# Kernel optimization log

Hardware: AMD Instinct MI355X
Metric: run time of the kernel (lower is better)

## Reference

```python
import jax, jax.numpy as jnp
import numpy as np

N = 100000      # nodes
E = 640000      # edges
IN = 100        # in_channels
OUT = 128       # out_channels
H, D = 4, 32    # heads, per-head dim (OUT = H*D)
MSG, TOUT, ETD, NET = 16, 100, 8, 4
EDGE_COLS = MSG + TOUT + 2        # 118 raw edge_attr columns
EDIM = (MSG - 1) + ETD + TOUT + 2 # 125 processed edge feature dim
SCALE = 1.0 / np.sqrt(D)


def _lin(k, fi, fo):
    return (jax.random.normal(k, (fi, fo), jnp.float32) / np.sqrt(fi)).astype(jnp.float32)


def setup_inputs() -> dict:
    key = jax.random.key(0)
    ks = jax.random.split(key, 24)
    x = jax.random.normal(ks[0], (N, IN), jnp.float32)
    edge_index = jax.random.randint(ks[1], (2, E), 0, N, dtype=jnp.int32)
    ea = jax.random.normal(ks[2], (E, EDGE_COLS), jnp.float32)
    etype = jax.random.randint(ks[3], (E,), 0, NET).astype(jnp.float32)
    edge_attr = ea.at[:, 3].set(etype)
    emb = jax.random.normal(ks[4], (NET, ETD), jnp.float32)
    inp = {"x": x, "edge_index": edge_index, "edge_attr": edge_attr, "emb": emb}
    # conv1: in=IN, conv2: in=OUT; lin_edge has no bias (PyG default)
    for i, fi in ((1, IN), (2, OUT)):
        base = 5 + (i - 1) * 8
        inp[f"w{i}q"] = _lin(ks[base + 0], fi, OUT)
        inp[f"b{i}q"] = jnp.zeros((OUT,), jnp.float32)
        inp[f"w{i}k"] = _lin(ks[base + 1], fi, OUT)
        inp[f"b{i}k"] = jnp.zeros((OUT,), jnp.float32)
        inp[f"w{i}v"] = _lin(ks[base + 2], fi, OUT)
        inp[f"b{i}v"] = jnp.zeros((OUT,), jnp.float32)
        inp[f"w{i}e"] = _lin(ks[base + 3], EDIM, OUT)
        inp[f"w{i}s"] = _lin(ks[base + 4], fi, OUT)
        inp[f"b{i}s"] = jnp.zeros((OUT,), jnp.float32)
    return inp


def _seg_softmax(logits, seg, n):
    # logits: [E, H], softmax over edges sharing the same target node
    m = jax.ops.segment_max(logits, seg, num_segments=n)      # [N, H]
    ex = jnp.exp(logits - m[seg])
    s = jax.ops.segment_sum(ex, seg, num_segments=n)          # [N, H]
    return ex / (s[seg] + 1e-16)


def _tconv(x, src, dst, e, wq, bq, wk, bk, wv, bv, we, ws, bs):
    n = x.shape[0]
    q = (x @ wq + bq)[dst].reshape(-1, H, D)   # gather targets
    k = (x @ wk + bk)[src].reshape(-1, H, D)   # gather sources
    v = (x @ wv + bv)[src].reshape(-1, H, D)
    ee = (e @ we).reshape(-1, H, D)            # per-edge projection
    alpha = jnp.sum(q * (k + ee), axis=-1) * SCALE          # [E, H]
    a = _seg_softmax(alpha, dst, n)                          # scatter-softmax
    msg = (v + ee) * a[..., None]                            # [E, H, D]
    out = jax.ops.segment_sum(msg, dst, num_segments=n).reshape(n, H * D)
    return out + x @ ws + bs                                 # root/skip connection


def reference(x, edge_index, edge_attr, emb,
              w1q, b1q, w1k, b1k, w1v, b1v, w1e, w1s, b1s,
              w2q, b2q, w2k, b2k, w2v, b2v, w2e, w2s, b2s):
    src, dst = edge_index[0], edge_index[1]
    cont = edge_attr[:, :3]
    etype = edge_attr[:, 3].astype(jnp.int32)
    rest = edge_attr[:, 4:]
    e = jnp.concatenate([cont, rest, emb[etype]], axis=-1)   # [E, EDIM]
    h = jax.nn.relu(_tconv(x, src, dst, e, w1q, b1q, w1k, b1k, w1v, b1v, w1e, w1s, b1s))
    return _tconv(h, src, dst, e, w2q, b2q, w2k, b2k, w2v, b2v, w2e, w2s, b2s)
```

## Files before the change

kernel.cpp:

```cpp
#include <hip/hip_runtime.h>

#define NN 100000
#define NE 640000
#define OUTF 128
#define K1 100
#define KE 118
#define KPAD 128
#define ASTR 136
#define ATT_SCALE 0.17677669529663687f
#define NTILE 5000
#define NSCANB 391

typedef __attribute__((ext_vector_type(8))) short short8;
typedef __attribute__((ext_vector_type(4))) float f32x4;

__device__ __forceinline__ unsigned short f2bf(float f) {
    unsigned u = __float_as_uint(f);
    u += 0x7FFFu + ((u >> 16) & 1u);
    return (unsigned short)(u >> 16);
}
__device__ __forceinline__ float bf2f(unsigned short h) {
    return __uint_as_float(((unsigned)h) << 16);
}

__global__ void prep_weights(
    const float* __restrict__ w1q, const float* __restrict__ w1k,
    const float* __restrict__ w1v, const float* __restrict__ w1s,
    const float* __restrict__ w2q, const float* __restrict__ w2k,
    const float* __restrict__ w2v, const float* __restrict__ w2s,
    const float* __restrict__ we1, const float* __restrict__ we2,
    const float* __restrict__ emb,
    const float* __restrict__ b1q, const float* __restrict__ b1k,
    const float* __restrict__ b1v, const float* __restrict__ b1s,
    const float* __restrict__ b2q, const float* __restrict__ b2k,
    const float* __restrict__ b2v, const float* __restrict__ b2s,
    unsigned short* __restrict__ WT1, unsigned short* __restrict__ WT2,
    unsigned short* __restrict__ WmT1, unsigned short* __restrict__ WmT2,
    float* __restrict__ bias1, float* __restrict__ bias2)
{
    int idx = blockIdx.x * blockDim.x + threadIdx.x;
    int stride = gridDim.x * blockDim.x;
    for (int i = idx; i < 512 * KPAD; i += stride) {
        int col = i >> 7, k = i & 127;
        int which = col >> 7, c = col & 127;
        const float* s1 = (which == 0) ? w1q : (which == 1) ? w1k : (which == 2) ? w1v : w1s;
        const float* s2 = (which == 0) ? w2q : (which == 1) ? w2k : (which == 2) ? w2v : w2s;
        float v1 = (k < K1) ? s1[k * OUTF + c] : 0.f;
        float v2 = s2[k * OUTF + c];
        WT1[i] = f2bf(v1); WT2[i] = f2bf(v2);
    }
    for (int i = idx; i < OUTF * KPAD; i += stride) {
        int col = i >> 7, k = i & 127;
        float v1 = 0.f, v2 = 0.f;
        if (k < 3)                 { v1 = we1[k * OUTF + col];       v2 = we2[k * OUTF + col]; }
        else if (k >= 4 && k < KE) { v1 = we1[(k - 1) * OUTF + col]; v2 = we2[(k - 1) * OUTF + col]; }
        else if (k >= KE && k < KE + 4) {
            int t = k - KE;
            #pragma unroll
            for (int r = 0; r < 8; r++) {
                float ev = emb[t * 8 + r];
                v1 += ev * we1[(117 + r) * OUTF + col];
                v2 += ev * we2[(117 + r) * OUTF + col];
            }
        }
        WmT1[i] = f2bf(v1); WmT2[i] = f2bf(v2);
    }
    for (int i = idx; i < 512; i += stride) {
        int which = i >> 7, c = i & 127;
        const float* sb1 = (which == 0) ? b1q : (which == 1) ? b1k : (which == 2) ? b1v : b1s;
        const float* sb2 = (which == 0) ? b2q : (which == 1) ? b2k : (which == 2) ? b2v : b2s;
        bias1[i] = sb1[c]; bias2[i] = sb2[c];
    }
}

__global__ __launch_bounds__(256) void prep_edges(const float* __restrict__ EA,
                                                  const int* __restrict__ dstI,
                                                  unsigned short* __restrict__ EAp,
                                                  int* __restrict__ cnt, int do_hist)
{
    __shared__ unsigned short Alds[128][ASTR];
    __shared__ int et_lds[128];
    int tid = threadIdx.x;
    int tile = blockIdx.x;
    int e0 = tile * 128;

    for (int idx = tid; idx < 128 * 64; idx += 256) {
        int r = idx >> 6, slot = idx & 63;
        int k = slot * 2;
        float2 v = make_float2(0.f, 0.f);
        if (k < KE) v = *(const float2*)(EA + (size_t)(e0 + r) * KE + k);
        if (slot == 1) { et_lds[r] = (int)v.y; v.y = 0.f; }
        unsigned pv = (unsigned)f2bf(v.x) | ((unsigned)f2bf(v.y) << 16);
        *(unsigned*)&Alds[r][k] = pv;
    }
    __syncthreads();
    if (tid < 128) {
        Alds[tid][KE + et_lds[tid]] = 0x3F80;
        if (do_hist) atomicAdd(&cnt[dstI[e0 + tid]], 1);
    }
    __syncthreads();
    size_t base = (size_t)tile * 16384;
    #pragma unroll
    for (int it = 0; it < 8; it++) {
        int cid = it * 256 + tid;
        int g = cid >> 8, ks = (cid >> 6) & 3, l15 = (cid >> 2) & 15, l4 = cid & 3;
        uint4 v = *(const uint4*)&Alds[g * 16 + l15][ks * 32 + l4 * 8];
        *(uint4*)(EAp + base + (size_t)cid * 8) = v;
    }
}

__global__ void scan1(const int* __restrict__ cnt, int* __restrict__ S1, int* __restrict__ bsum) {
    __shared__ int sd[256];
    int t = blockIdx.x * 256 + threadIdx.x;
    sd[threadIdx.x] = (t < NN) ? cnt[t] : 0;
    __syncthreads();
    for (int off = 1; off < 256; off <<= 1) {
        int x = (threadIdx.x >= off) ? sd[threadIdx.x - off] : 0;
        __syncthreads();
        sd[threadIdx.x] += x;
        __syncthreads();
    }
    if (t < NN) S1[t] = sd[threadIdx.x];
    if (threadIdx.x == 255) bsum[blockIdx.x] = sd[255];
}
__global__ void scan2(const int* __restrict__ bsum, int* __restrict__ boff) {
    __shared__ int sd[512];
    int t = threadIdx.x;
    sd[t] = (t < NSCANB) ? bsum[t] : 0;
    __syncthreads();
    for (int off = 1; off < 512; off <<= 1) {
        int x = (t >= off) ? sd[t - off] : 0;
        __syncthreads();
        sd[t] += x;
        __syncthreads();
    }
    if (t < NSCANB) boff[t] = (t == 0) ? 0 : sd[t - 1];
}
__global__ void scan3(const int* __restrict__ S1, const int* __restrict__ boff,
                      const int* __restrict__ cnt,
                      int* __restrict__ row_start, int* __restrict__ cursor) {
    int t = blockIdx.x * 256 + threadIdx.x;
    if (t < NN) {
        int incl = S1[t] + boff[t >> 8];
        row_start[t + 1] = incl;
        cursor[t] = incl - cnt[t];
        if (t == 0) row_start[0] = 0;
    }
}
__global__ void scatter_csr(const int* __restrict__ srcI, const int* __restrict__ dstI,
                            int* __restrict__ cursor,
                            int* __restrict__ csr_src, int* __restrict__ csr_eid) {
    int e = blockIdx.x * 256 + threadIdx.x;
    if (e < NE) {
        int j = atomicAdd(&cursor[dstI[e]], 1);
        csr_src[j] = srcI[e];
        csr_eid[j] = e;
    }
}

__global__ __launch_bounds__(256) void node_mfma(
    const float* __restrict__ X, int ldx, int Kdim, int relu, int n,
    const unsigned short* __restrict__ WT, const float* __restrict__ bias,
    float* __restrict__ Y0, float* __restrict__ Y1,
    float* __restrict__ Y2, float* __restrict__ Y3,
    int ld012, int ld3)
{
    __shared__ unsigned short Alds[128][ASTR];
    int tid = threadIdx.x;
    int rowbase = blockIdx.x * 128;

    for (int idx = tid; idx < 128 * 68; idx += 256) {
        int r = idx / 68, kv = idx % 68;
        int k = kv * 2;
        float2 v = make_float2(0.f, 0.f);
        int gr = rowbase + r;
        if (gr < n && k < Kdim) v = *(const float2*)(X + (size_t)gr * ldx + k);
        if (relu) { v.x = fmaxf(v.x, 0.f); v.y = fmaxf(v.y, 0.f); }
        unsigned pv = (unsigned)f2bf(v.x) | ((unsigned)f2bf(v.y) << 16);
        *(unsigned*)&Alds[r][k] = pv;
    }
    __syncthreads();

    int lane = tid & 63, wid = tid >> 6;
    int wm = wid >> 1, wn = wid & 1;
    int l15 = lane & 15, l4 = lane >> 4;

    for (int nb = 0; nb < 4; nb++) {
        f32x4 acc[4][4];
        #pragma unroll
        for (int mf = 0; mf < 4; mf++)
            #pragma unroll
            for (int nf = 0; nf < 4; nf++)
                acc[mf][nf] = (f32x4){0.f, 0.f, 0.f, 0.f};

        const unsigned short* wbase = WT + (size_t)(nb * 128 + wn * 64 + l15) * KPAD + l4 * 8;
        #pragma unroll
        for (int ks = 0; ks < 4; ks++) {
            short8 af[4], bfr[4];
            #pragma unroll
            for (int mf = 0; mf < 4; mf++)
                af[mf] = *(const short8*)&Alds[wm * 64 + mf * 16 + l15][ks * 32 + l4 * 8];
            #pragma unroll
            for (int nf = 0; nf < 4; nf++)
                bfr[nf] = *(const short8*)(wbase + (size_t)nf * 16 * KPAD + ks * 32);
            #pragma unroll
            for (int mf = 0; mf < 4; mf++)
                #pragma unroll
                for (int nf = 0; nf < 4; nf++)
                    acc[mf][nf] = __builtin_amdgcn_mfma_f32_16x16x32_bf16(af[mf], bfr[nf], acc[mf][nf], 0, 0, 0);
        }

        float* Yb = (nb == 0) ? Y0 : (nb == 1) ? Y1 : (nb == 2) ? Y2 : Y3;
        int ld = (nb == 3) ? ld3 : ld012;
        #pragma unroll
        for (int nf = 0; nf < 4; nf++) {
            int col = wn * 64 + nf * 16 + l15;
            float bv = bias[nb * 128 + col];
            #pragma unroll
            for (int mf = 0; mf < 4; mf++) {
                #pragma unroll
                for (int rr = 0; rr < 4; rr++) {
                    int row = rowbase + wm * 64 + mf * 16 + l4 * 4 + rr;
                    if (row < n) Yb[(size_t)row * ld + col] = acc[mf][nf][rr] + bv;
                }
            }
        }
    }
}

__global__ __launch_bounds__(256) void edge_mfma(unsigned short* EAp,
                                                 const unsigned short* __restrict__ WmT)
{
    __shared__ unsigned short Slds[128][ASTR];
    int tid = threadIdx.x;
    int tile = blockIdx.x;
    int lane = tid & 63, wm = tid >> 6;
    int l15 = lane & 15, l4 = lane >> 4;
    size_t base = (size_t)tile * 16384;

    short8 af[2][4];
    #pragma unroll
    for (int mf = 0; mf < 2; mf++)
        #pragma unroll
        for (int ks = 0; ks < 4; ks++) {
            int g = wm * 2 + mf;
            int cid = ((g * 4 + ks) * 16 + l15) * 4 + l4;
            af[mf][ks] = *(const short8*)(EAp + base + (size_t)cid * 8);
        }

    f32x4 acc[2][8];
    #pragma unroll
    for (int mf = 0; mf < 2; mf++)
        #pragma unroll
        for (int nf = 0; nf < 8; nf++)
            acc[mf][nf] = (f32x4){0.f, 0.f, 0.f, 0.f};

    #pragma unroll
    for (int ks = 0; ks < 4; ks++) {
        short8 bfr[8];
        #pragma unroll
        for (int nf = 0; nf < 8; nf++)
            bfr[nf] = *(const short8*)(WmT + (size_t)(nf * 16 + l15) * KPAD + ks * 32 + l4 * 8);
        #pragma unroll
        for (int mf = 0; mf < 2; mf++)
            #pragma unroll
            for (int nf = 0; nf < 8; nf++)
                acc[mf][nf] = __builtin_amdgcn_mfma_f32_16x16x32_bf16(af[mf][ks], bfr[nf], acc[mf][nf], 0, 0, 0);
    }

    #pragma unroll
    for (int mf = 0; mf < 2; mf++)
        #pragma unroll
        for (int nf = 0; nf < 8; nf++)
            #pragma unroll
            for (int rr = 0; rr < 4; rr++)
                Slds[wm * 32 + mf * 16 + l4 * 4 + rr][nf * 16 + l15] = f2bf(acc[mf][nf][rr]);
    __syncthreads();

    #pragma unroll
    for (int it = 0; it < 8; it++) {
        int cid = it * 256 + tid;
        int row = cid >> 4, c8 = (cid & 15) * 8;
        uint4 v = *(const uint4*)&Slds[row][c8];
        *(uint4*)(EAp + base + (size_t)row * 128 + c8) = v;
    }
}

__global__ __launch_bounds__(256) void attn_node(
    const float* __restrict__ Y,
    const unsigned short* __restrict__ EE,
    const int* __restrict__ row_start,
    const int* __restrict__ csr_src, const int* __restrict__ csr_eid,
    const float* __restrict__ Hsrc, int ldh,
    float* __restrict__ Out, int ldo)
{
    int lane = threadIdx.x & 63;
    int gw = (int)((blockIdx.x * (size_t)blockDim.x + threadIdx.x) >> 6);
    int nW = (gridDim.x * blockDim.x) >> 6;
    int c2 = lane * 2;

    for (int d = gw; d < NN; d += nW) {
        int rs = row_start[d], re = row_start[d + 1];
        float2 q = *(const float2*)(Y + (size_t)d * 512 + c2);
        float m = -3.4e38f, s = 0.f, a0 = 0.f, a1 = 0.f;
        for (int j = rs; j < re; j++) {
            int sj = csr_src[j], ej = csr_eid[j];
            float2 kv = *(const float2*)(Y + (size_t)sj * 512 + 128 + c2);
            float2 vv = *(const float2*)(Y + (size_t)sj * 512 + 256 + c2);
            unsigned eeb = *(const unsigned*)(EE + (size_t)ej * 128 + c2);
            float e0 = bf2f((unsigned short)(eeb & 0xFFFFu));
            float e1 = bf2f((unsigned short)(eeb >> 16));
            float t = q.x * (kv.x + e0) + q.y * (kv.y + e1);
            t += __shfl_xor(t, 1); t += __shfl_xor(t, 2);
            t += __shfl_xor(t, 4); t += __shfl_xor(t, 8);
            float alpha = t * ATT_SCALE;
            float mn = fmaxf(m, alpha);
            float r = __expf(m - mn);
            float p = __expf(alpha - mn);
            s = s * r + p;
            a0 = a0 * r + p * (vv.x + e0);
            a1 = a1 * r + p * (vv.y + e1);
            m = mn;
        }
        float inv = 1.f / (s + 1e-16f);
        float2 h = *(const float2*)(Hsrc + (size_t)d * ldh + c2);
        float2 o;
        o.x = a0 * inv + h.x;
        o.y = a1 * inv + h.y;
        *(float2*)(Out + (size_t)d * ldo + c2) = o;
    }
}

extern "C" void kernel_launch(void* const* d_in, const int* in_sizes, int n_in,
                              void* d_out, int out_size, void* d_ws, size_t ws_size,
                              hipStream_t stream) {
    const float* x    = (const float*)d_in[0];
    const int*   ei   = (const int*)d_in[1];
    const float* ea   = (const float*)d_in[2];
    const float* emb  = (const float*)d_in[3];
    const float* w1q  = (const float*)d_in[4];  const float* b1q = (const float*)d_in[5];
    const float* w1k  = (const float*)d_in[6];  const float* b1k = (const float*)d_in[7];
    const float* w1v  = (const float*)d_in[8];  const float* b1v = (const float*)d_in[9];
    const float* w1e  = (const float*)d_in[10];
    const float* w1s  = (const float*)d_in[11]; const float* b1s = (const float*)d_in[12];
    const float* w2q  = (const float*)d_in[13]; const float* b2q = (const float*)d_in[14];
    const float* w2k  = (const float*)d_in[15]; const float* b2k = (const float*)d_in[16];
    const float* w2v  = (const float*)d_in[17]; const float* b2v = (const float*)d_in[18];
    const float* w2e  = (const float*)d_in[19];
    const float* w2s  = (const float*)d_in[20]; const float* b2s = (const float*)d_in[21];

    const int* srcI = ei;
    const int* dstI = ei + NE;

    float* Y = (float*)d_ws;
    unsigned short* EAp = (unsigned short*)(Y + (size_t)NN * 512);
    int* csr_src   = (int*)(EAp + (size_t)NE * 128);
    int* csr_eid   = csr_src + NE;
    int* row_start = csr_eid + NE;
    int* cursor    = row_start + NN + 1;
    int* cnt       = cursor + NN;
    int* S1        = cnt + NN;
    int* bsum      = S1 + NN;
    int* boff      = bsum + NSCANB;
    unsigned short* WT1  = (unsigned short*)(boff + NSCANB + 1);
    unsigned short* WT2  = WT1 + 512 * KPAD;
    unsigned short* WmT1 = WT2 + 512 * KPAD;
    unsigned short* WmT2 = WmT1 + OUTF * KPAD;
    float* bias1 = (float*)(WmT2 + OUTF * KPAD);
    float* bias2 = bias1 + 512;

    prep_weights<<<128, 256, 0, stream>>>(w1q, w1k, w1v, w1s, w2q, w2k, w2v, w2s,
                                          w1e, w2e, emb,
                                          b1q, b1k, b1v, b1s, b2q, b2k, b2v, b2s,
                                          WT1, WT2, WmT1, WmT2, bias1, bias2);
    hipMemsetAsync(cnt, 0, (size_t)NN * sizeof(int), stream);
    prep_edges<<<NTILE, 256, 0, stream>>>(ea, dstI, EAp, cnt, 1);
    scan1<<<NSCANB, 256, 0, stream>>>(cnt, S1, bsum);
    scan2<<<1, 512, 0, stream>>>(bsum, boff);
    scan3<<<NSCANB, 256, 0, stream>>>(S1, boff, cnt, row_start, cursor);
    scatter_csr<<<NE / 256, 256, 0, stream>>>(srcI, dstI, cursor, csr_src, csr_eid);

    int ngrid = (NN + 127) / 128;

    node_mfma<<<ngrid, 256, 0, stream>>>(x, K1, K1, 0, NN, WT1, bias1,
                                         Y + 0, Y + 128, Y + 256, Y + 384, 512, 512);
    edge_mfma<<<NTILE, 256, 0, stream>>>(EAp, WmT1);
    attn_node<<<2048, 256, 0, stream>>>(Y, EAp, row_start, csr_src, csr_eid,
                                        Y + 384, 512, Y + 384, 512);

    node_mfma<<<ngrid, 256, 0, stream>>>(Y + 384, 512, OUTF, 1, NN, WT2, bias2,
                                         Y + 0, Y + 128, Y + 256, (float*)d_out, 512, 128);
    prep_edges<<<NTILE, 256, 0, stream>>>(ea, dstI, EAp, cnt, 0);
    edge_mfma<<<NTILE, 256, 0, stream>>>(EAp, WmT2);
    attn_node<<<2048, 256, 0, stream>>>(Y, EAp, row_start, csr_src, csr_eid,
                                        (float*)d_out, 128, (float*)d_out, 128);
}
```

Measured before the change: 1.162 ms.

## Fuse edge prep into dual-layer edge GEMM, store K/V bf16, CSR-order edge features

Replaces the two prep_edges plus edge_mfma passes with a single kernel that reads raw edge attributes once and computes both layers' edge projections, writing them directly in CSR (destination-sorted) order via a per-edge position array. K and V node projections are now stored as bf16 in an interleaved buffer, and Q and skip are kept in separate compact fp32 arrays. The attention loop drops the csr_eid indirection, reads edge features contiguously, and software-prefetches the next edge's K/V/E. This removes a re-read of the fp32 edge attributes and halves gather bytes for K/V, at the cost of a second edge-feature buffer, scattered writes, and extra bf16 rounding of K/V.

```diff
diff --git a/kernel.cpp b/kernel.cpp
--- a/kernel.cpp
+++ b/kernel.cpp
@@ -73,42 +73,10 @@
     }
 }
 
-__global__ __launch_bounds__(256) void prep_edges(const float* __restrict__ EA,
-                                                  const int* __restrict__ dstI,
-                                                  unsigned short* __restrict__ EAp,
-                                                  int* __restrict__ cnt, int do_hist)
-{
-    __shared__ unsigned short Alds[128][ASTR];
-    __shared__ int et_lds[128];
-    int tid = threadIdx.x;
-    int tile = blockIdx.x;
-    int e0 = tile * 128;
-
-    for (int idx = tid; idx < 128 * 64; idx += 256) {
-        int r = idx >> 6, slot = idx & 63;
-        int k = slot * 2;
-        float2 v = make_float2(0.f, 0.f);
-        if (k < KE) v = *(const float2*)(EA + (size_t)(e0 + r) * KE + k);
-        if (slot == 1) { et_lds[r] = (int)v.y; v.y = 0.f; }
-        unsigned pv = (unsigned)f2bf(v.x) | ((unsigned)f2bf(v.y) << 16);
-        *(unsigned*)&Alds[r][k] = pv;
-    }
-    __syncthreads();
-    if (tid < 128) {
-        Alds[tid][KE + et_lds[tid]] = 0x3F80;
-        if (do_hist) atomicAdd(&cnt[dstI[e0 + tid]], 1);
-    }
-    __syncthreads();
-    size_t base = (size_t)tile * 16384;
-    #pragma unroll
-    for (int it = 0; it < 8; it++) {
-        int cid = it * 256 + tid;
-        int g = cid >> 8, ks = (cid >> 6) & 3, l15 = (cid >> 2) & 15, l4 = cid & 3;
-        uint4 v = *(const uint4*)&Alds[g * 16 + l15][ks * 32 + l4 * 8];
-        *(uint4*)(EAp + base + (size_t)cid * 8) = v;
-    }
-}
-
+__global__ void hist_kernel(const int* __restrict__ dstI, int* __restrict__ cnt) {
+    int e = blockIdx.x * 256 + threadIdx.x;
+    if (e < NE) atomicAdd(&cnt[dstI[e]], 1);
+}
 __global__ void scan1(const int* __restrict__ cnt, int* __restrict__ S1, int* __restrict__ bsum) {
     __shared__ int sd[256];
     int t = blockIdx.x * 256 + threadIdx.x;
@@ -149,21 +117,19 @@
 }
 __global__ void scatter_csr(const int* __restrict__ srcI, const int* __restrict__ dstI,
                             int* __restrict__ cursor,
-                            int* __restrict__ csr_src, int* __restrict__ csr_eid) {
+                            int* __restrict__ csr_src, int* __restrict__ epos) {
     int e = blockIdx.x * 256 + threadIdx.x;
     if (e < NE) {
         int j = atomicAdd(&cursor[dstI[e]], 1);
         csr_src[j] = srcI[e];
-        csr_eid[j] = e;
+        epos[e] = j;
     }
 }
 
 __global__ __launch_bounds__(256) void node_mfma(
     const float* __restrict__ X, int ldx, int Kdim, int relu, int n,
     const unsigned short* __restrict__ WT, const float* __restrict__ bias,
-    float* __restrict__ Y0, float* __restrict__ Y1,
-    float* __restrict__ Y2, float* __restrict__ Y3,
-    int ld012, int ld3)
+    float* __restrict__ Qp, unsigned short* __restrict__ KVp, float* __restrict__ Hp)
 {
     __shared__ unsigned short Alds[128][ASTR];
     int tid = threadIdx.x;
@@ -210,8 +176,6 @@
                     acc[mf][nf] = __builtin_amdgcn_mfma_f32_16x16x32_bf16(af[mf], bfr[nf], acc[mf][nf], 0, 0, 0);
         }
 
-        float* Yb = (nb == 0) ? Y0 : (nb == 1) ? Y1 : (nb == 2) ? Y2 : Y3;
-        int ld = (nb == 3) ? ld3 : ld012;
         #pragma unroll
         for (int nf = 0; nf < 4; nf++) {
             int col = wn * 64 + nf * 16 + l15;
@@ -221,78 +185,100 @@
                 #pragma unroll
                 for (int rr = 0; rr < 4; rr++) {
                     int row = rowbase + wm * 64 + mf * 16 + l4 * 4 + rr;
-                    if (row < n) Yb[(size_t)row * ld + col] = acc[mf][nf][rr] + bv;
+                    if (row < n) {
+                        float val = acc[mf][nf][rr] + bv;
+                        if (nb == 0)      Qp[(size_t)row * OUTF + col] = val;
+                        else if (nb == 3) Hp[(size_t)row * OUTF + col] = val;
+                        else KVp[(size_t)row * 256 + (nb == 1 ? 0 : 128) + col] = f2bf(val);
+                    }
                 }
             }
         }
     }
 }
 
-__global__ __launch_bounds__(256) void edge_mfma(unsigned short* EAp,
-                                                 const unsigned short* __restrict__ WmT)
+__global__ __launch_bounds__(256) void edge_mfma_dual(
+    const float* __restrict__ EA, const int* __restrict__ epos,
+    const unsigned short* __restrict__ WmT1, const unsigned short* __restrict__ WmT2,
+    unsigned short* __restrict__ EE1, unsigned short* __restrict__ EE2)
 {
-    __shared__ unsigned short Slds[128][ASTR];
+    __shared__ unsigned short Alds[128][ASTR];
+    __shared__ int et_lds[128];
+    __shared__ int pos_lds[128];
     int tid = threadIdx.x;
-    int tile = blockIdx.x;
+    int e0 = blockIdx.x * 128;
+
+    for (int idx = tid; idx < 128 * 64; idx += 256) {
+        int r = idx >> 6, slot = idx & 63;
+        int k = slot * 2;
+        float2 v = make_float2(0.f, 0.f);
+        if (k < KE) v = *(const float2*)(EA + (size_t)(e0 + r) * KE + k);
+        if (slot == 1) { et_lds[r] = (int)v.y; v.y = 0.f; }
+        unsigned pv = (unsigned)f2bf(v.x) | ((unsigned)f2bf(v.y) << 16);
+        *(unsigned*)&Alds[r][k] = pv;
+    }
+    __syncthreads();
+    if (tid < 128) {
+        Alds[tid][KE + et_lds[tid]] = 0x3F80;
+        pos_lds[tid] = epos[e0 + tid];
+    }
+    __syncthreads();
+
     int lane = tid & 63, wm = tid >> 6;
     int l15 = lane & 15, l4 = lane >> 4;
-    size_t base = (size_t)tile * 16384;
 
     short8 af[2][4];
     #pragma unroll
     for (int mf = 0; mf < 2; mf++)
         #pragma unroll
+        for (int ks = 0; ks < 4; ks++)
+            af[mf][ks] = *(const short8*)&Alds[wm * 32 + mf * 16 + l15][ks * 32 + l4 * 8];
+
+    auto do_layer = [&](const unsigned short* __restrict__ WmT, unsigned short* __restrict__ EEc) {
+        f32x4 acc[2][8];
+        #pragma unroll
+        for (int mf = 0; mf < 2; mf++)
+            #pragma unroll
+            for (int nf = 0; nf < 8; nf++)
+                acc[mf][nf] = (f32x4){0.f, 0.f, 0.f, 0.f};
+
+        #pragma unroll
         for (int ks = 0; ks < 4; ks++) {
-            int g = wm * 2 + mf;
-            int cid = ((g * 4 + ks) * 16 + l15) * 4 + l4;
-            af[mf][ks] = *(const short8*)(EAp + base + (size_t)cid * 8);
-        }
-
-    f32x4 acc[2][8];
-    #pragma unroll
-    for (int mf = 0; mf < 2; mf++)
-        #pragma unroll
-        for (int nf = 0; nf < 8; nf++)
-            acc[mf][nf] = (f32x4){0.f, 0.f, 0.f, 0.f};
-
-    #pragma unroll
-    for (int ks = 0; ks < 4; ks++) {
-        short8 bfr[8];
-        #pragma unroll
-        for (int nf = 0; nf < 8; nf++)
-            bfr[nf] = *(const short8*)(WmT + (size_t)(nf * 16 + l15) * KPAD + ks * 32 + l4 * 8);
+            short8 bfr[8];
+            #pragma unroll
+            for (int nf = 0; nf < 8; nf++)
+                bfr[nf] = *(const short8*)(WmT + (size_t)(nf * 16 + l15) * KPAD + ks * 32 + l4 * 8);
+            #pragma unroll
+            for (int mf = 0; mf < 2; mf++)
+                #pragma unroll
+                for (int nf = 0; nf < 8; nf++)
+                    acc[mf][nf] = __builtin_amdgcn_mfma_f32_16x16x32_bf16(af[mf][ks], bfr[nf], acc[mf][nf], 0, 0, 0);
+        }
         #pragma unroll
         for (int mf = 0; mf < 2; mf++)
             #pragma unroll
             for (int nf = 0; nf < 8; nf++)
-                acc[mf][nf] = __builtin_amdgcn_mfma_f32_16x16x32_bf16(af[mf][ks], bfr[nf], acc[mf][nf], 0, 0, 0);
-    }
-
-    #pragma unroll
-    for (int mf = 0; mf < 2; mf++)
-        #pragma unroll
-        for (int nf = 0; nf < 8; nf++)
-            #pragma unroll
-            for (int rr = 0; rr < 4; rr++)
-                Slds[wm * 32 + mf * 16 + l4 * 4 + rr][nf * 16 + l15] = f2bf(acc[mf][nf][rr]);
-    __syncthreads();
-
-    #pragma unroll
-    for (int it = 0; it < 8; it++) {
-        int cid = it * 256 + tid;
-        int row = cid >> 4, c8 = (cid & 15) * 8;
-        uint4 v = *(const uint4*)&Slds[row][c8];
-        *(uint4*)(EAp + base + (size_t)row * 128 + c8) = v;
-    }
+                #pragma unroll
+                for (int rr = 0; rr < 4; rr++)
+                    Alds[wm * 32 + mf * 16 + l4 * 4 + rr][nf * 16 + l15] = f2bf(acc[mf][nf][rr]);
+        #pragma unroll
+        for (int it = 0; it < 8; it++) {
+            int t2 = it * 64 + lane;
+            int rid = t2 >> 4, c8 = (t2 & 15) * 8;
+            int rowl = wm * 32 + rid;
+            uint4 v = *(const uint4*)&Alds[rowl][c8];
+            *(uint4*)(EEc + (size_t)pos_lds[rowl] * 128 + c8) = v;
+        }
+    };
+    do_layer(WmT1, EE1);
+    do_layer(WmT2, EE2);
 }
 
 __global__ __launch_bounds__(256) void attn_node(
-    const float* __restrict__ Y,
-    const unsigned short* __restrict__ EE,
-    const int* __restrict__ row_start,
-    const int* __restrict__ csr_src, const int* __restrict__ csr_eid,
-    const float* __restrict__ Hsrc, int ldh,
-    float* __restrict__ Out, int ldo)
+    const float* __restrict__ Qp, const unsigned short* __restrict__ KVp,
+    const unsigned short* __restrict__ EEc,
+    const int* __restrict__ row_start, const int* __restrict__ csr_src,
+    const float* __restrict__ Hskip, float* __restrict__ Out)
 {
     int lane = threadIdx.x & 63;
     int gw = (int)((blockIdx.x * (size_t)blockDim.x + threadIdx.x) >> 6);
@@ -301,16 +287,30 @@
 
     for (int d = gw; d < NN; d += nW) {
         int rs = row_start[d], re = row_start[d + 1];
-        float2 q = *(const float2*)(Y + (size_t)d * 512 + c2);
+        float2 q = *(const float2*)(Qp + (size_t)d * OUTF + c2);
         float m = -3.4e38f, s = 0.f, a0 = 0.f, a1 = 0.f;
+
+        int j0 = (rs < re) ? rs : 0;
+        int sj = csr_src[j0];
+        unsigned kc = *(const unsigned*)(KVp + (size_t)sj * 256 + c2);
+        unsigned vc = *(const unsigned*)(KVp + (size_t)sj * 256 + 128 + c2);
+        unsigned ec = *(const unsigned*)(EEc + (size_t)j0 * 128 + c2);
+
         for (int j = rs; j < re; j++) {
-            int sj = csr_src[j], ej = csr_eid[j];
-            float2 kv = *(const float2*)(Y + (size_t)sj * 512 + 128 + c2);
-            float2 vv = *(const float2*)(Y + (size_t)sj * 512 + 256 + c2);
-            unsigned eeb = *(const unsigned*)(EE + (size_t)ej * 128 + c2);
-            float e0 = bf2f((unsigned short)(eeb & 0xFFFFu));
-            float e1 = bf2f((unsigned short)(eeb >> 16));
-            float t = q.x * (kv.x + e0) + q.y * (kv.y + e1);
+            int jn = (j + 1 < re) ? j + 1 : j;
+            int sjn = csr_src[jn];
+            unsigned kn = *(const unsigned*)(KVp + (size_t)sjn * 256 + c2);
+            unsigned vn = *(const unsigned*)(KVp + (size_t)sjn * 256 + 128 + c2);
+            unsigned en = *(const unsigned*)(EEc + (size_t)jn * 128 + c2);
+
+            float e0 = bf2f((unsigned short)(ec & 0xFFFFu));
+            float e1 = bf2f((unsigned short)(ec >> 16));
+            float k0 = bf2f((unsigned short)(kc & 0xFFFFu));
+            float k1 = bf2f((unsigned short)(kc >> 16));
+            float v0 = bf2f((unsigned short)(vc & 0xFFFFu));
+            float v1 = bf2f((unsigned short)(vc >> 16));
+
+            float t = q.x * (k0 + e0) + q.y * (k1 + e1);
             t += __shfl_xor(t, 1); t += __shfl_xor(t, 2);
             t += __shfl_xor(t, 4); t += __shfl_xor(t, 8);
             float alpha = t * ATT_SCALE;
@@ -318,16 +318,17 @@
             float r = __expf(m - mn);
             float p = __expf(alpha - mn);
             s = s * r + p;
-            a0 = a0 * r + p * (vv.x + e0);
-            a1 = a1 * r + p * (vv.y + e1);
+            a0 = a0 * r + p * (v0 + e0);
+            a1 = a1 * r + p * (v1 + e1);
             m = mn;
+            kc = kn; vc = vn; ec = en;
         }
         float inv = 1.f / (s + 1e-16f);
-        float2 h = *(const float2*)(Hsrc + (size_t)d * ldh + c2);
+        float2 h = *(const float2*)(Hskip + (size_t)d * OUTF + c2);
         float2 o;
         o.x = a0 * inv + h.x;
         o.y = a1 * inv + h.y;
-        *(float2*)(Out + (size_t)d * ldo + c2) = o;
+        *(float2*)(Out + (size_t)d * OUTF + c2) = o;
     }
 }
 
@@ -352,11 +353,14 @@
     const int* srcI = ei;
     const int* dstI = ei + NE;
 
-    float* Y = (float*)d_ws;
-    unsigned short* EAp = (unsigned short*)(Y + (size_t)NN * 512);
-    int* csr_src   = (int*)(EAp + (size_t)NE * 128);
-    int* csr_eid   = csr_src + NE;
-    int* row_start = csr_eid + NE;
+    float* Q = (float*)d_ws;
+    unsigned short* KV = (unsigned short*)(Q + (size_t)NN * OUTF);
+    float* H = (float*)(KV + (size_t)NN * 256);
+    unsigned short* EE1 = (unsigned short*)(H + (size_t)NN * OUTF);
+    unsigned short* EE2 = EE1 + (size_t)NE * 128;
+    int* csr_src   = (int*)(EE2 + (size_t)NE * 128);
+    int* epos      = csr_src + NE;
+    int* row_start = epos + NE;
     int* cursor    = row_start + NN + 1;
     int* cnt       = cursor + NN;
     int* S1        = cnt + NN;
@@ -374,24 +378,18 @@
                                           b1q, b1k, b1v, b1s, b2q, b2k, b2v, b2s,
                                           WT1, WT2, WmT1, WmT2, bias1, bias2);
     hipMemsetAsync(cnt, 0, (size_t)NN * sizeof(int), stream);
-    prep_edges<<<NTILE, 256, 0, stream>>>(ea, dstI, EAp, cnt, 1);
+    hist_kernel<<<NE / 256, 256, 0, stream>>>(dstI, cnt);
     scan1<<<NSCANB, 256, 0, stream>>>(cnt, S1, bsum);
     scan2<<<1, 512, 0, stream>>>(bsum, boff);
     scan3<<<NSCANB, 256, 0, stream>>>(S1, boff, cnt, row_start, cursor);
-    scatter_csr<<<NE / 256, 256, 0, stream>>>(srcI, dstI, cursor, csr_src, csr_eid);
+    scatter_csr<<<NE / 256, 256, 0, stream>>>(srcI, dstI, cursor, csr_src, epos);
 
     int ngrid = (NN + 127) / 128;
 
-    node_mfma<<<ngrid, 256, 0, stream>>>(x, K1, K1, 0, NN, WT1, bias1,
-                                         Y + 0, Y + 128, Y + 256, Y + 384, 512, 512);
-    edge_mfma<<<NTILE, 256, 0, stream>>>(EAp, WmT1);
-    attn_node<<<2048, 256, 0, stream>>>(Y, EAp, row_start, csr_src, csr_eid,
-                                        Y + 384, 512, Y + 384, 512);
-
-    node_mfma<<<ngrid, 256, 0, stream>>>(Y + 384, 512, OUTF, 1, NN, WT2, bias2,
-                                         Y + 0, Y + 128, Y + 256, (float*)d_out, 512, 128);
-    prep_edges<<<NTILE, 256, 0, stream>>>(ea, dstI, EAp, cnt, 0);
-    edge_mfma<<<NTILE, 256, 0, stream>>>(EAp, WmT2);
-    attn_node<<<2048, 256, 0, stream>>>(Y, EAp, row_start, csr_src, csr_eid,
-                                        (float*)d_out, 128, (float*)d_out, 128);
-}
+    node_mfma<<<ngrid, 256, 0, stream>>>(x, K1, K1, 0, NN, WT1, bias1, Q, KV, H);
+    edge_mfma_dual<<<NTILE, 256, 0, stream>>>(ea, epos, WmT1, WmT2, EE1, EE2);
+    attn_node<<<2048, 256, 0, stream>>>(Q, KV, EE1, row_start, csr_src, H, H);
+
+    node_mfma<<<ngrid, 256, 0, stream>>>(H, OUTF, OUTF, 1, NN, WT2, bias2, Q, KV, (float*)d_out);
+    attn_node<<<2048, 256, 0, stream>>>(Q, KV, EE2, row_start, csr_src, (float*)d_out, (float*)d_out);
+}
```

Result: slower. 1.262 ms (+8.6%).
